# Optimization experiments

Hardware: AMD Instinct MI355X
Metric: run time of the kernel (lower is better)

The kernel has to match this reference:

```python
import jax, jax.numpy as jnp
import numpy as np

D_MODEL = 1024
N_HEADS = 16
D_HEAD = D_MODEL // N_HEADS


def setup_inputs() -> dict:
    key = jax.random.key(0)
    k1, k2, k3, k4, k5, k6 = jax.random.split(key, 6)
    B, Q, T = 4, 1024, 4096
    s = 1.0 / np.sqrt(D_MODEL)  # ~ kaiming-uniform scale for Linear weights
    return {
        "q_in": jax.random.normal(k1, (B, Q, D_MODEL), dtype=jnp.float32),
        "kv_in": jax.random.normal(k2, (B, T, D_MODEL), dtype=jnp.float32),
        "Wq": jax.random.normal(k3, (D_MODEL, D_MODEL), dtype=jnp.float32) * s,
        "Wk": jax.random.normal(k4, (D_MODEL, D_MODEL), dtype=jnp.float32) * s,
        "Wv": jax.random.normal(k5, (D_MODEL, D_MODEL), dtype=jnp.float32) * s,
        "Wo": jax.random.normal(k6, (D_MODEL, D_MODEL), dtype=jnp.float32) * s,
    }


def reference(q_in, kv_in, Wq, Wk, Wv, Wo):
    B, Q, D = q_in.shape
    T = kv_in.shape[1]
    scale = D_HEAD ** -0.5
    # projections; torch Linear: y = x @ W.T
    q = (q_in @ Wq.T).reshape(B, Q, N_HEADS, D_HEAD)
    k = (kv_in @ Wk.T).reshape(B, T, N_HEADS, D_HEAD)
    v = (kv_in @ Wv.T).reshape(B, T, N_HEADS, D_HEAD)
    # scores [B, H, Q, T]
    w = jnp.einsum("bqhd,bthd->bhqt", q, k) * scale
    w = jax.nn.softmax(w.astype(jnp.float32), axis=-1).astype(q.dtype)
    # dropout p=0.0 -> identity
    out = jnp.einsum("bhqt,bthd->bqhd", w, v).reshape(B, Q, D)
    return out @ Wo.T
```

## Files before the change

### kernel.cpp

```cpp
#include <hip/hip_runtime.h>
#include <hip/hip_bf16.h>
#include <cstdint>
#include <cstddef>

#define DM 1024
#define NH 16
#define DH 64
#define BQ 1024
#define TT 4096
#define BB 4
#define NSPLIT 2
#define TSPLIT (TT / NSPLIT)

using f32x4 = __attribute__((ext_vector_type(4))) float;
using f32x16 = __attribute__((ext_vector_type(16))) float;
using s16x8 = __attribute__((ext_vector_type(8))) short;

__device__ __forceinline__ unsigned short f2bf(float f) {
  union { __hip_bfloat16 h; unsigned short u; } c;
  c.h = __float2bfloat16(f);
  return c.u;
}

__device__ __forceinline__ float exp2_raw(float x) {
  return __builtin_amdgcn_exp2f(x);
}

__device__ __forceinline__ f32x16 fill16(float v) {
  f32x16 z;
#pragma unroll
  for (int i = 0; i < 16; i++) z[i] = v;
  return z;
}

__device__ __forceinline__ int pack2(float lo, float hi2) {
  return (int)((unsigned int)f2bf(lo) | ((unsigned int)f2bf(hi2) << 16));
}

template<int RB>
__device__ __forceinline__ s16x8 mkfrag(const f32x16& p, int hi) {
  const int W1 = pack2(p[RB + 0], p[RB + 1]);
  const int W3 = pack2(p[RB + 2], p[RB + 3]);
  const int W2 = pack2(p[RB + 4], p[RB + 5]);
  const int W4 = pack2(p[RB + 6], p[RB + 7]);
  const int s1 = __shfl_xor(W1, 32);
  const int s3 = __shfl_xor(W3, 32);
  const int s2 = __shfl_xor(W2, 32);
  const int s4 = __shfl_xor(W4, 32);
  union { int i[4]; s16x8 v; } u;
  u.i[0] = hi ? s2 : W1;
  u.i[1] = hi ? s4 : W3;
  u.i[2] = hi ? W2 : s1;
  u.i[3] = hi ? W4 : s3;
  return u.v;
}

__global__ void cvt_f32_bf16(const float* __restrict__ in, unsigned short* __restrict__ out, int n4) {
  int i = blockIdx.x * blockDim.x + threadIdx.x;
  if (i < n4) {
    float4 v = reinterpret_cast<const float4*>(in)[i];
    ushort4 o;
    o.x = f2bf(v.x); o.y = f2bf(v.y); o.z = f2bf(v.z); o.w = f2bf(v.w);
    reinterpret_cast<ushort4*>(out)[i] = o;
  }
}

__global__ void cvt_w4(const float* __restrict__ w0, const float* __restrict__ w1,
                       const float* __restrict__ w2, const float* __restrict__ w3,
                       unsigned short* __restrict__ o0, unsigned short* __restrict__ o1,
                       unsigned short* __restrict__ o2, unsigned short* __restrict__ o3,
                       int n4) {
  int i = blockIdx.x * blockDim.x + threadIdx.x;
  if (i >= n4) return;
  const float* in; unsigned short* out;
  switch (blockIdx.y) {
    case 0: in = w0; out = o0; break;
    case 1: in = w1; out = o1; break;
    case 2: in = w2; out = o2; break;
    default: in = w3; out = o3; break;
  }
  float4 v = reinterpret_cast<const float4*>(in)[i];
  ushort4 o;
  o.x = f2bf(v.x); o.y = f2bf(v.y); o.z = f2bf(v.z); o.w = f2bf(v.w);
  reinterpret_cast<ushort4*>(out)[i] = o;
}

__device__ __forceinline__ void gload_lds16(const unsigned short* g, unsigned short* l) {
  __builtin_amdgcn_global_load_lds(
      (const __attribute__((address_space(1))) unsigned int*)g,
      (__attribute__((address_space(3))) unsigned int*)l,
      16, 0, 0);
}

__device__ __forceinline__ int xcd_swz(int lin, int nwg) {
  return (lin & 7) * (nwg >> 3) + (lin >> 3);
}

template<int MODE, int SEQ, bool PRESCALE, int NT>
__global__ __launch_bounds__(256) void gemm_bt(const unsigned short* __restrict__ A,
                                               const unsigned short* __restrict__ W,
                                               unsigned short* __restrict__ Cb,
                                               float* __restrict__ Cf) {
  __shared__ unsigned short As[128 * 32];
  __shared__ unsigned short Bs[128 * 32];
  const int tid = threadIdx.x;
  const int wid = tid >> 6, lane = tid & 63;
  const int swz = xcd_swz(blockIdx.x, gridDim.x);
  const int m0 = (swz / NT) * 128, n0 = (swz % NT) * 128;
  const int wr = wid >> 1, wc = wid & 1;
  const int fr = lane & 15;
  const int fk = (lane >> 4) * 8;

  f32x4 acc[4][4];
#pragma unroll
  for (int mt = 0; mt < 4; mt++)
#pragma unroll
    for (int nt = 0; nt < 4; nt++) acc[mt][nt] = f32x4{0.f, 0.f, 0.f, 0.f};

  const unsigned short* gA = A + (size_t)(m0 + wid * 32 + (lane >> 2)) * DM + (lane & 3) * 8;
  const unsigned short* gW = W + (size_t)(n0 + wid * 32 + (lane >> 2)) * DM + (lane & 3) * 8;
  unsigned short* lA0 = &As[(wid * 32) * 32];
  unsigned short* lA1 = &As[(wid * 32 + 16) * 32];
  unsigned short* lB0 = &Bs[(wid * 32) * 32];
  unsigned short* lB1 = &Bs[(wid * 32 + 16) * 32];

  for (int kt = 0; kt < DM / 32; ++kt) {
    gload_lds16(gA, lA0);
    gload_lds16(gA + 16 * DM, lA1);
    gload_lds16(gW, lB0);
    gload_lds16(gW + 16 * DM, lB1);
    gA += 32; gW += 32;
    __syncthreads();
    s16x8 af[4], bfv[4];
#pragma unroll
    for (int mt = 0; mt < 4; mt++)
      af[mt] = *reinterpret_cast<const s16x8*>(&As[(wr * 64 + mt * 16 + fr) * 32 + fk]);
#pragma unroll
    for (int nt = 0; nt < 4; nt++)
      bfv[nt] = *reinterpret_cast<const s16x8*>(&Bs[(wc * 64 + nt * 16 + fr) * 32 + fk]);
    __builtin_amdgcn_s_setprio(1);
#pragma unroll
    for (int mt = 0; mt < 4; mt++)
#pragma unroll
      for (int nt = 0; nt < 4; nt++)
        acc[mt][nt] = __builtin_amdgcn_mfma_f32_16x16x32_bf16(af[mt], bfv[nt], acc[mt][nt], 0, 0, 0);
    __builtin_amdgcn_s_setprio(0);
    __syncthreads();
  }

#pragma unroll
  for (int mt = 0; mt < 4; mt++) {
#pragma unroll
    for (int nt = 0; nt < 4; nt++) {
      const int col = n0 + wc * 64 + nt * 16 + fr;
#pragma unroll
      for (int r = 0; r < 4; r++) {
        const int m = m0 + wr * 64 + mt * 16 + (lane >> 4) * 4 + r;
        float v = acc[mt][nt][r];
        if constexpr (PRESCALE) v *= 0.18033688011112042f;
        if constexpr (MODE == 0) {
          const int b = m / SEQ, sr = m % SEQ;
          const int h = col >> 6, dh = col & 63;
          Cb[((size_t)(b * NH + h) * SEQ + sr) * DH + dh] = f2bf(v);
        } else {
          Cf[(size_t)m * DM + col] = v;
        }
      }
    }
  }
}

__global__ __launch_bounds__(256) void gemm_kv(const unsigned short* __restrict__ A,
                                               const unsigned short* __restrict__ Wkv,
                                               unsigned short* __restrict__ Kp,
                                               unsigned short* __restrict__ Vt) {
  __shared__ unsigned short As[128 * 32];
  __shared__ unsigned short Bs[128 * 32];
  const int tid = threadIdx.x;
  const int wid = tid >> 6, lane = tid & 63;
  const int swz = xcd_swz(blockIdx.x, gridDim.x);
  const int m0 = (swz >> 4) * 128, n0 = (swz & 15) * 128;
  const int wr = wid >> 1, wc = wid & 1;
  const int fr = lane & 15;
  const int fk = (lane >> 4) * 8;

  f32x4 acc[4][4];
#pragma unroll
  for (int mt = 0; mt < 4; mt++)
#pragma unroll
    for (int nt = 0; nt < 4; nt++) acc[mt][nt] = f32x4{0.f, 0.f, 0.f, 0.f};

  const unsigned short* gA = A + (size_t)(m0 + wid * 32 + (lane >> 2)) * DM + (lane & 3) * 8;
  const unsigned short* gW = Wkv + (size_t)(n0 + wid * 32 + (lane >> 2)) * DM + (lane & 3) * 8;
  unsigned short* lA0 = &As[(wid * 32) * 32];
  unsigned short* lA1 = &As[(wid * 32 + 16) * 32];
  unsigned short* lB0 = &Bs[(wid * 32) * 32];
  unsigned short* lB1 = &Bs[(wid * 32 + 16) * 32];

  for (int kt = 0; kt < DM / 32; ++kt) {
    gload_lds16(gA, lA0);
    gload_lds16(gA + 16 * DM, lA1);
    gload_lds16(gW, lB0);
    gload_lds16(gW + 16 * DM, lB1);
    gA += 32; gW += 32;
    __syncthreads();
    s16x8 af[4], bfv[4];
#pragma unroll
    for (int mt = 0; mt < 4; mt++)
      af[mt] = *reinterpret_cast<const s16x8*>(&As[(wr * 64 + mt * 16 + fr) * 32 + fk]);
#pragma unroll
    for (int nt = 0; nt < 4; nt++)
      bfv[nt] = *reinterpret_cast<const s16x8*>(&Bs[(wc * 64 + nt * 16 + fr) * 32 + fk]);
    __builtin_amdgcn_s_setprio(1);
#pragma unroll
    for (int mt = 0; mt < 4; mt++)
#pragma unroll
      for (int nt = 0; nt < 4; nt++)
        acc[mt][nt] = __builtin_amdgcn_mfma_f32_16x16x32_bf16(af[mt], bfv[nt], acc[mt][nt], 0, 0, 0);
    __builtin_amdgcn_s_setprio(0);
    __syncthreads();
  }

  const int klg = lane >> 4;
#pragma unroll
  for (int mt = 0; mt < 4; mt++) {
#pragma unroll
    for (int nt = 0; nt < 4; nt++) {
      const int col = n0 + wc * 64 + nt * 16 + fr;
      const int tb = m0 + wr * 64 + mt * 16 + klg * 4;
      const int b = tb >> 12, sr = tb & (TT - 1);
      if (col < DM) {
        const int h = col >> 6, dh = col & 63;
#pragma unroll
        for (int r = 0; r < 4; r++)
          Kp[((size_t)(b * NH + h) * TT + sr + r) * DH + dh] = f2bf(acc[mt][nt][r]);
      } else {
        const int c2 = col - DM;
        const int h = c2 >> 6, dh = c2 & 63;
        ushort4 pk;
        pk.x = f2bf(acc[mt][nt][0]);
        pk.y = f2bf(acc[mt][nt][1]);
        pk.z = f2bf(acc[mt][nt][2]);
        pk.w = f2bf(acc[mt][nt][3]);
        *reinterpret_cast<ushort4*>(&Vt[((size_t)(b * NH + h) * DH + dh) * TT + sr]) = pk;
      }
    }
  }
}

#define ATTN_TILE(CUR, DO_STAGE, SBUF)                                             \
  do {                                                                             \
    if (DO_STAGE) {                                                                \
      gload_lds16(gK, &KVs[(SBUF)][wid * 512]);                                    \
      gload_lds16(gV, &KVs[2 + (SBUF)][wid * 512]);                                \
      gK += 64 * DH; gV += 64;                                                     \
    }                                                                              \
    f32x16 s0 = fill16(-7.0f), s1 = fill16(-7.0f);                                 \
    __builtin_amdgcn_s_setprio(1);                                                 \
    _Pragma("unroll")                                                              \
    for (int kk = 0; kk < 4; kk++) {                                               \
      s16x8 kb0 = *reinterpret_cast<const s16x8*>(lds0 + (CUR) * 8192 + offA[kk]); \
      s0 = __builtin_amdgcn_mfma_f32_32x32x16_bf16(kb0, qf[kk], s0, 0, 0, 0);      \
      s16x8 kb1 = *reinterpret_cast<const s16x8*>(lds0 + (CUR) * 8192 + offB[kk]); \
      s1 = __builtin_amdgcn_mfma_f32_32x32x16_bf16(kb1, qf[kk], s1, 0, 0, 0);      \
    }                                                                              \
    __builtin_amdgcn_s_setprio(0);                                                 \
    _Pragma("unroll")                                                              \
    for (int r = 0; r < 16; r++) {                                                 \
      s0[r] = exp2_raw(s0[r]); lsum += s0[r];                                      \
      s1[r] = exp2_raw(s1[r]); lsum += s1[r];                                      \
    }                                                                              \
    s16x8 pa[4];                                                                   \
    pa[0] = mkfrag<0>(s0, hi);                                                     \
    pa[1] = mkfrag<8>(s0, hi);                                                     \
    pa[2] = mkfrag<0>(s1, hi);                                                     \
    pa[3] = mkfrag<8>(s1, hi);                                                     \
    __builtin_amdgcn_s_setprio(1);                                                 \
    _Pragma("unroll")                                                              \
    for (int kk = 0; kk < 4; kk++) {                                               \
      s16x8 vb0 = *reinterpret_cast<const s16x8*>(lds0 + 16384 + (CUR) * 8192 + offA[kk]); \
      o0 = __builtin_amdgcn_mfma_f32_32x32x16_bf16(pa[kk], vb0, o0, 0, 0, 0);      \
      s16x8 vb1 = *reinterpret_cast<const s16x8*>(lds0 + 16384 + (CUR) * 8192 + offB[kk]); \
      o1 = __builtin_amdgcn_mfma_f32_32x32x16_bf16(pa[kk], vb1, o1, 0, 0, 0);      \
    }                                                                              \
    __builtin_amdgcn_s_setprio(0);                                                 \
    __syncthreads();                                                               \
  } while (0)

__global__ __launch_bounds__(512, 4) void attn_kern(const unsigned short* __restrict__ Qp,
                                                    const unsigned short* __restrict__ Kp,
                                                    const unsigned short* __restrict__ Vtg,
                                                    float* __restrict__ Opart,
                                                    float* __restrict__ lsums) {
  __shared__ unsigned short KVs[4][64 * 64];
  const int bh = blockIdx.x;
  const int q0 = blockIdx.y * 256;
  const int split = blockIdx.z;
  const int t00 = split * TSPLIT;
  const int tid = threadIdx.x, wid = tid >> 6, lane = tid & 63;
  const int l31 = lane & 31, hi = lane >> 5;

  const size_t qrow = (size_t)bh * BQ + q0 + wid * 32 + l31;
  s16x8 qf[4];
#pragma unroll
  for (int kk = 0; kk < 4; kk++)
    qf[kk] = *reinterpret_cast<const s16x8*>(&Qp[qrow * DH + 16 * kk + 8 * hi]);

  f32x16 o0 = fill16(0.f), o1 = fill16(0.f);
  float lsum = 0.f;

  const size_t kvbase = (size_t)bh * TT * DH;
  const int rk = tid >> 3;
  const int c8 = tid & 7;

  const unsigned short* gK = Kp + kvbase + (size_t)(t00 + rk) * DH + (c8 ^ (rk & 7)) * 8;
  const unsigned short* gV = Vtg + kvbase + (size_t)rk * TT + t00 + (c8 ^ (rk & 7)) * 8;

  const char* lds0 = (const char*)&KVs[0][0];
  const int sw = l31 & 7;
  int offA[4], offB[4];
#pragma unroll
  for (int kk = 0; kk < 4; kk++) {
    offA[kk] = (l31 * 64 + (((2 * kk + hi) ^ sw) * 8)) * 2;
    offB[kk] = ((32 + l31) * 64 + (((2 * kk + hi) ^ sw) * 8)) * 2;
  }

  gload_lds16(gK, &KVs[0][wid * 512]);
  gload_lds16(gV, &KVs[2][wid * 512]);
  gK += 64 * DH; gV += 64;
  __syncthreads();

  const int NIT = TSPLIT / 128;
  for (int it2 = 0; it2 < NIT; ++it2) {
    ATTN_TILE(0, true, 1);
    ATTN_TILE(1, (it2 < NIT - 1), 0);
  }

  lsum += __shfl_xor(lsum, 32);
  if (lane < 32)
    lsums[((size_t)split * (BB * NH) + bh) * BQ + q0 + wid * 32 + lane] = lsum;

#pragma unroll
  for (int r = 0; r < 16; r++) {
    const int q = (r & 3) + 8 * (r >> 2) + 4 * hi;
    const size_t orow = (((size_t)split * (BB * NH) + bh) * BQ + q0 + wid * 32 + q) * DH;
    Opart[orow + l31] = o0[r];
    Opart[orow + 32 + l31] = o1[r];
  }
}

__global__ __launch_bounds__(256) void attn_combine(const float* __restrict__ Opart,
                                                    const float* __restrict__ lsums,
                                                    unsigned short* __restrict__ Ob) {
  const int gid = blockIdx.x * 256 + threadIdx.x;
  const int row = gid >> 4, seg = gid & 15;
  float denom = 0.f;
#pragma unroll
  for (int s = 0; s < NSPLIT; s++) denom += lsums[(size_t)s * (BB * NH * BQ) + row];
  const float inv = 1.0f / denom;
  float4 acc = {0.f, 0.f, 0.f, 0.f};
#pragma unroll
  for (int s = 0; s < NSPLIT; s++) {
    const float4 p = reinterpret_cast<const float4*>(Opart)[(size_t)s * (BB * NH * BQ) * 16 + (size_t)row * 16 + seg];
    acc.x += p.x; acc.y += p.y; acc.z += p.z; acc.w += p.w;
  }
  const int bh = row >> 10, q = row & (BQ - 1);
  const int b = bh >> 4, h = bh & 15;
  ushort4 o;
  o.x = f2bf(acc.x * inv);
  o.y = f2bf(acc.y * inv);
  o.z = f2bf(acc.z * inv);
  o.w = f2bf(acc.w * inv);
  *reinterpret_cast<ushort4*>(&Ob[((size_t)b * BQ + q) * DM + h * DH + seg * 4]) = o;
}

extern "C" void kernel_launch(void* const* d_in, const int* in_sizes, int n_in,
                              void* d_out, int out_size, void* d_ws, size_t ws_size,
                              hipStream_t stream) {
  const float* q_in = (const float*)d_in[0];
  const float* kv_in = (const float*)d_in[1];
  const float* Wq = (const float*)d_in[2];
  const float* Wk = (const float*)d_in[3];
  const float* Wv = (const float*)d_in[4];
  const float* Wo = (const float*)d_in[5];
  float* out = (float*)d_out;

  char* ws = (char*)d_ws;
  unsigned short* qin_b = (unsigned short*)ws;  ws += (size_t)BB * BQ * DM * 2;
  unsigned short* kvin_b = (unsigned short*)ws; ws += (size_t)BB * TT * DM * 2;
  unsigned short* Wq_b = (unsigned short*)ws;   ws += (size_t)DM * DM * 2;
  unsigned short* Wk_b = (unsigned short*)ws;   ws += (size_t)DM * DM * 2;
  unsigned short* Wv_b = (unsigned short*)ws;   ws += (size_t)DM * DM * 2;
  unsigned short* Wo_b = (unsigned short*)ws;   ws += (size_t)DM * DM * 2;
  unsigned short* qp = (unsigned short*)ws;     ws += (size_t)BB * NH * BQ * DH * 2;
  unsigned short* kp = (unsigned short*)ws;     ws += (size_t)BB * NH * TT * DH * 2;
  unsigned short* vt = (unsigned short*)ws;     ws += (size_t)BB * NH * DH * TT * 2;
  unsigned short* ao = (unsigned short*)ws;     ws += (size_t)BB * BQ * DM * 2;
  float* Opart = (float*)ws;                    ws += (size_t)NSPLIT * BB * NH * BQ * DH * 4;
  float* lsums = (float*)ws;                    ws += (size_t)NSPLIT * BB * NH * BQ * 4;

  const int qn4 = BB * BQ * DM / 4;
  const int kvn4 = BB * TT * DM / 4;
  const int wn4 = DM * DM / 4;
  cvt_f32_bf16<<<(qn4 + 255) / 256, 256, 0, stream>>>(q_in, qin_b, qn4);
  cvt_f32_bf16<<<(kvn4 + 255) / 256, 256, 0, stream>>>(kv_in, kvin_b, kvn4);
  cvt_w4<<<dim3((wn4 + 255) / 256, 4), 256, 0, stream>>>(Wq, Wk, Wv, Wo,
                                                         Wq_b, Wk_b, Wv_b, Wo_b, wn4);

  dim3 blk(256);
  gemm_bt<0, BQ, true, 8><<<dim3(BB * BQ / 128 * 8), blk, 0, stream>>>(qin_b, Wq_b, qp, nullptr);
  gemm_kv<<<dim3(BB * TT / 128 * 16), blk, 0, stream>>>(kvin_b, Wk_b, kp, vt);

  attn_kern<<<dim3(BB * NH, BQ / 256, NSPLIT), dim3(512), 0, stream>>>(qp, kp, vt, Opart, lsums);
  attn_combine<<<dim3(BB * NH * BQ * 16 / 256), blk, 0, stream>>>(Opart, lsums, ao);

  gemm_bt<1, BQ, false, 8><<<dim3(BB * BQ / 128 * 8), blk, 0, stream>>>(ao, Wo_b, nullptr, out);
}
```

Baseline: 262.3 us.

## Double-buffer GEMM LDS tiles with BK=64 and XOR-swizzled layout

The projection GEMMs move from a single-buffered 32-wide K tile to double-buffered 64-wide K tiles. Global-to-LDS loads for the next tile are issued before the MFMAs on the current one, and there are half as many barriers. An XOR swizzle on the 16-byte column chunks is meant to cut LDS bank conflicts on the fragment reads. LDS use grows from 16 KB to 64 KB per block, which may lower occupancy.

```diff
diff --git a/kernel.cpp b/kernel.cpp
--- a/kernel.cpp
+++ b/kernel.cpp
@@ -96,20 +96,59 @@
   return (lin & 7) * (nwg >> 3) + (lin >> 3);
 }
 
+
+#define GEMM_STAGE(AS, BS, BUF)                                              \
+  do {                                                                       \
+    _Pragma("unroll")                                                        \
+    for (int s = 0; s < 4; s++) {                                            \
+      gload_lds16(gA + (size_t)(s * 8) * DM, &AS[BUF][(wid * 32 + s * 8) * 64]); \
+      gload_lds16(gW + (size_t)(s * 8) * DM, &BS[BUF][(wid * 32 + s * 8) * 64]); \
+    }                                                                        \
+    gA += 64; gW += 64;                                                      \
+  } while (0)
+
+#define GEMM_COMPUTE(AS, BS, BUF)                                            \
+  do {                                                                       \
+    __builtin_amdgcn_s_setprio(1);                                           \
+    _Pragma("unroll")                                                        \
+    for (int kk = 0; kk < 2; kk++) {                                         \
+      s16x8 af[4], bfv[4];                                                   \
+      _Pragma("unroll")                                                      \
+      for (int mt = 0; mt < 4; mt++) {                                       \
+        const int row = wr * 64 + mt * 16 + fr;                              \
+        af[mt] = *reinterpret_cast<const s16x8*>(                            \
+            &AS[BUF][row * 64 + (((kk * 4 + fkg) ^ (fr & 7)) * 8)]);         \
+      }                                                                      \
+      _Pragma("unroll")                                                      \
+      for (int nt = 0; nt < 4; nt++) {                                       \
+        const int row = wc * 64 + nt * 16 + fr;                              \
+        bfv[nt] = *reinterpret_cast<const s16x8*>(                           \
+            &BS[BUF][row * 64 + (((kk * 4 + fkg) ^ (fr & 7)) * 8)]);         \
+      }                                                                      \
+      _Pragma("unroll")                                                      \
+      for (int mt = 0; mt < 4; mt++)                                         \
+        _Pragma("unroll")                                                    \
+        for (int nt = 0; nt < 4; nt++)                                       \
+          acc[mt][nt] = __builtin_amdgcn_mfma_f32_16x16x32_bf16(             \
+              af[mt], bfv[nt], acc[mt][nt], 0, 0, 0);                        \
+    }                                                                        \
+    __builtin_amdgcn_s_setprio(0);                                           \
+  } while (0)
+
 template<int MODE, int SEQ, bool PRESCALE, int NT>
 __global__ __launch_bounds__(256) void gemm_bt(const unsigned short* __restrict__ A,
                                                const unsigned short* __restrict__ W,
                                                unsigned short* __restrict__ Cb,
                                                float* __restrict__ Cf) {
-  __shared__ unsigned short As[128 * 32];
-  __shared__ unsigned short Bs[128 * 32];
+  __shared__ unsigned short As[2][128 * 64];
+  __shared__ unsigned short Bs[2][128 * 64];
   const int tid = threadIdx.x;
   const int wid = tid >> 6, lane = tid & 63;
   const int swz = xcd_swz(blockIdx.x, gridDim.x);
   const int m0 = (swz / NT) * 128, n0 = (swz % NT) * 128;
   const int wr = wid >> 1, wc = wid & 1;
   const int fr = lane & 15;
-  const int fk = (lane >> 4) * 8;
+  const int fkg = lane >> 4;
 
   f32x4 acc[4][4];
 #pragma unroll
@@ -117,34 +156,19 @@
 #pragma unroll
     for (int nt = 0; nt < 4; nt++) acc[mt][nt] = f32x4{0.f, 0.f, 0.f, 0.f};
 
-  const unsigned short* gA = A + (size_t)(m0 + wid * 32 + (lane >> 2)) * DM + (lane & 3) * 8;
-  const unsigned short* gW = W + (size_t)(n0 + wid * 32 + (lane >> 2)) * DM + (lane & 3) * 8;
-  unsigned short* lA0 = &As[(wid * 32) * 32];
-  unsigned short* lA1 = &As[(wid * 32 + 16) * 32];
-  unsigned short* lB0 = &Bs[(wid * 32) * 32];
-  unsigned short* lB1 = &Bs[(wid * 32 + 16) * 32];
-
-  for (int kt = 0; kt < DM / 32; ++kt) {
-    gload_lds16(gA, lA0);
-    gload_lds16(gA + 16 * DM, lA1);
-    gload_lds16(gW, lB0);
-    gload_lds16(gW + 16 * DM, lB1);
-    gA += 32; gW += 32;
+  const int srow = lane >> 3;
+  const int sc8 = (lane & 7) ^ (srow & 7);
+  const unsigned short* gA = A + (size_t)(m0 + wid * 32 + srow) * DM + sc8 * 8;
+  const unsigned short* gW = W + (size_t)(n0 + wid * 32 + srow) * DM + sc8 * 8;
+
+  GEMM_STAGE(As, Bs, 0);
+  __syncthreads();
+  for (int kt = 0; kt < DM / 64; kt += 2) {
+    if (kt + 1 < DM / 64) GEMM_STAGE(As, Bs, 1);
+    GEMM_COMPUTE(As, Bs, 0);
     __syncthreads();
-    s16x8 af[4], bfv[4];
-#pragma unroll
-    for (int mt = 0; mt < 4; mt++)
-      af[mt] = *reinterpret_cast<const s16x8*>(&As[(wr * 64 + mt * 16 + fr) * 32 + fk]);
-#pragma unroll
-    for (int nt = 0; nt < 4; nt++)
-      bfv[nt] = *reinterpret_cast<const s16x8*>(&Bs[(wc * 64 + nt * 16 + fr) * 32 + fk]);
-    __builtin_amdgcn_s_setprio(1);
-#pragma unroll
-    for (int mt = 0; mt < 4; mt++)
-#pragma unroll
-      for (int nt = 0; nt < 4; nt++)
-        acc[mt][nt] = __builtin_amdgcn_mfma_f32_16x16x32_bf16(af[mt], bfv[nt], acc[mt][nt], 0, 0, 0);
-    __builtin_amdgcn_s_setprio(0);
+    if (kt + 2 < DM / 64) GEMM_STAGE(As, Bs, 0);
+    GEMM_COMPUTE(As, Bs, 1);
     __syncthreads();
   }
 
@@ -174,15 +198,15 @@
                                                const unsigned short* __restrict__ Wkv,
                                                unsigned short* __restrict__ Kp,
                                                unsigned short* __restrict__ Vt) {
-  __shared__ unsigned short As[128 * 32];
-  __shared__ unsigned short Bs[128 * 32];
+  __shared__ unsigned short As[2][128 * 64];
+  __shared__ unsigned short Bs[2][128 * 64];
   const int tid = threadIdx.x;
   const int wid = tid >> 6, lane = tid & 63;
   const int swz = xcd_swz(blockIdx.x, gridDim.x);
   const int m0 = (swz >> 4) * 128, n0 = (swz & 15) * 128;
   const int wr = wid >> 1, wc = wid & 1;
   const int fr = lane & 15;
-  const int fk = (lane >> 4) * 8;
+  const int fkg = lane >> 4;
 
   f32x4 acc[4][4];
 #pragma unroll
@@ -190,34 +214,19 @@
 #pragma unroll
     for (int nt = 0; nt < 4; nt++) acc[mt][nt] = f32x4{0.f, 0.f, 0.f, 0.f};
 
-  const unsigned short* gA = A + (size_t)(m0 + wid * 32 + (lane >> 2)) * DM + (lane & 3) * 8;
-  const unsigned short* gW = Wkv + (size_t)(n0 + wid * 32 + (lane >> 2)) * DM + (lane & 3) * 8;
-  unsigned short* lA0 = &As[(wid * 32) * 32];
-  unsigned short* lA1 = &As[(wid * 32 + 16) * 32];
-  unsigned short* lB0 = &Bs[(wid * 32) * 32];
-  unsigned short* lB1 = &Bs[(wid * 32 + 16) * 32];
-
-  for (int kt = 0; kt < DM / 32; ++kt) {
-    gload_lds16(gA, lA0);
-    gload_lds16(gA + 16 * DM, lA1);
-    gload_lds16(gW, lB0);
-    gload_lds16(gW + 16 * DM, lB1);
-    gA += 32; gW += 32;
+  const int srow = lane >> 3;
+  const int sc8 = (lane & 7) ^ (srow & 7);
+  const unsigned short* gA = A + (size_t)(m0 + wid * 32 + srow) * DM + sc8 * 8;
+  const unsigned short* gW = Wkv + (size_t)(n0 + wid * 32 + srow) * DM + sc8 * 8;
+
+  GEMM_STAGE(As, Bs, 0);
+  __syncthreads();
+  for (int kt = 0; kt < DM / 64; kt += 2) {
+    if (kt + 1 < DM / 64) GEMM_STAGE(As, Bs, 1);
+    GEMM_COMPUTE(As, Bs, 0);
     __syncthreads();
-    s16x8 af[4], bfv[4];
-#pragma unroll
-    for (int mt = 0; mt < 4; mt++)
-      af[mt] = *reinterpret_cast<const s16x8*>(&As[(wr * 64 + mt * 16 + fr) * 32 + fk]);
-#pragma unroll
-    for (int nt = 0; nt < 4; nt++)
-      bfv[nt] = *reinterpret_cast<const s16x8*>(&Bs[(wc * 64 + nt * 16 + fr) * 32 + fk]);
-    __builtin_amdgcn_s_setprio(1);
-#pragma unroll
-    for (int mt = 0; mt < 4; mt++)
-#pragma unroll
-      for (int nt = 0; nt < 4; nt++)
-        acc[mt][nt] = __builtin_amdgcn_mfma_f32_16x16x32_bf16(af[mt], bfv[nt], acc[mt][nt], 0, 0, 0);
-    __builtin_amdgcn_s_setprio(0);
+    if (kt + 2 < DM / 64) GEMM_STAGE(As, Bs, 0);
+    GEMM_COMPUTE(As, Bs, 1);
     __syncthreads();
   }
 
```

After: 243.7 us. -7.1%, faster.
